# Performance work log

Hardware: AMD Instinct MI355X
Metric: run time of the kernel (lower is better)

## Reference

```python
import jax, jax.numpy as jnp
import numpy as np

B, LAT, H, OUT, S, L = 256, 128, 256, 64, 512, 2


def _lstm_layer(xs, h0, c0, Wih, Whh, bih, bhh):
    # xs: [B, S, in_dim]; PyTorch gate order i, f, g, o
    gx = jnp.einsum('bsi,gi->bsg', xs, Wih) + bih + bhh  # [B,S,4H], precomputed input proj
    gx = jnp.swapaxes(gx, 0, 1)  # [S,B,4H]

    def step(carry, g_t):
        h, c = carry
        g = g_t + h @ Whh.T
        i, f, gg, o = jnp.split(g, 4, axis=-1)
        i, f, o = jax.nn.sigmoid(i), jax.nn.sigmoid(f), jax.nn.sigmoid(o)
        c = f * c + i * jnp.tanh(gg)
        h = o * jnp.tanh(c)
        return (h, c), h

    (_, _), hs = jax.lax.scan(step, (h0, c0), gx)
    return jnp.swapaxes(hs, 0, 1)  # [B,S,H]


def setup_inputs() -> dict:
    key = jax.random.key(0)
    ks = jax.random.split(key, 20)
    sc = 0.05
    d = {
        'z': jax.random.normal(ks[0], (B, LAT), jnp.float32),
        'fc_hidden_w': jax.random.normal(ks[1], (H * L, LAT), jnp.float32) * sc,
        'fc_hidden_b': jnp.zeros((H * L,), jnp.float32),
        'fc_cell_w': jax.random.normal(ks[2], (H * L, LAT), jnp.float32) * sc,
        'fc_cell_b': jnp.zeros((H * L,), jnp.float32),
        'fc_input_w': jax.random.normal(ks[3], (H, LAT), jnp.float32) * sc,
        'fc_input_b': jnp.zeros((H,), jnp.float32),
        'W_ih0': jax.random.normal(ks[4], (4 * H, H), jnp.float32) * sc,
        'W_hh0': jax.random.normal(ks[5], (4 * H, H), jnp.float32) * sc,
        'b_ih0': jnp.zeros((4 * H,), jnp.float32),
        'b_hh0': jnp.zeros((4 * H,), jnp.float32),
        'W_ih1': jax.random.normal(ks[6], (4 * H, H), jnp.float32) * sc,
        'W_hh1': jax.random.normal(ks[7], (4 * H, H), jnp.float32) * sc,
        'b_ih1': jnp.zeros((4 * H,), jnp.float32),
        'b_hh1': jnp.zeros((4 * H,), jnp.float32),
        'fc_output_w': jax.random.normal(ks[8], (OUT, H), jnp.float32) * sc,
        'fc_output_b': jnp.zeros((OUT,), jnp.float32),
    }
    return d


def reference(z, fc_hidden_w, fc_hidden_b, fc_cell_w, fc_cell_b, fc_input_w, fc_input_b,
              W_ih0, W_hh0, b_ih0, b_hh0, W_ih1, W_hh1, b_ih1, b_hh1,
              fc_output_w, fc_output_b):
    # init hidden/cell per layer: view(B, L, H) -> layer axis first
    hidden = (z @ fc_hidden_w.T + fc_hidden_b).reshape(B, L, H)
    cell = (z @ fc_cell_w.T + fc_cell_b).reshape(B, L, H)
    # repeated decoder input (same vector at every timestep)
    x0 = z @ fc_input_w.T + fc_input_b  # [B,H]
    xs = jnp.broadcast_to(x0[:, None, :], (B, S, H))
    h1 = _lstm_layer(xs, hidden[:, 0], cell[:, 0], W_ih0, W_hh0, b_ih0, b_hh0)
    # dropout between layers is inference no-op
    h2 = _lstm_layer(h1, hidden[:, 1], cell[:, 1], W_ih1, W_hh1, b_ih1, b_hh1)
    return h2 @ fc_output_w.T + fc_output_b  # [B,S,OUT]
```

## Files before the change

kernel.cpp:

```cpp
#include <hip/hip_runtime.h>
#include <hip/hip_bf16.h>

#define LAT 128
#define H 256
#define OUTD 64
#define SEQ 512

typedef short bf16x8 __attribute__((ext_vector_type(8)));
typedef float f32x4  __attribute__((ext_vector_type(4)));
typedef unsigned long long u64;
typedef unsigned u32;

__device__ __forceinline__ float sigm(float x)  { return 1.f / (1.f + __expf(-x)); }
__device__ __forceinline__ float tanhf_(float x){ return 1.f - 2.f / (__expf(2.f * x) + 1.f); }

__device__ __forceinline__ short f2bs(float x) {
    __hip_bfloat16 b = __float2bfloat16(x);
    return *reinterpret_cast<short*>(&b);
}
__device__ __forceinline__ float bs2f(unsigned short h) {
    u32 b = ((u32)h) << 16;
    float f; __builtin_memcpy(&f, &b, 4); return f;
}
__device__ __forceinline__ u32 f2pair(float a, float b) {
    return ((u32)(unsigned short)f2bs(b) << 16) | (u32)(unsigned short)f2bs(a);
}
__device__ __forceinline__ bf16x8 pack8(const float* s) {
    bf16x8 v;
    v[0]=f2bs(s[0]); v[1]=f2bs(s[1]); v[2]=f2bs(s[2]); v[3]=f2bs(s[3]);
    v[4]=f2bs(s[4]); v[5]=f2bs(s[5]); v[6]=f2bs(s[6]); v[7]=f2bs(s[7]);
    return v;
}

__device__ __forceinline__ u64 sys_load_u64(const u64* p) {
    return __hip_atomic_load((u64*)p, __ATOMIC_RELAXED, __HIP_MEMORY_SCOPE_AGENT);
}
__device__ __forceinline__ void sys_store_u64(u64* p, u64 v) {
    __hip_atomic_store(p, v, __ATOMIC_RELAXED, __HIP_MEMORY_SCOPE_AGENT);
}

__global__ void lstm_prologue_init(const float* __restrict__ z,
                                   const float* __restrict__ Whid,
                                   const float* __restrict__ bhid,
                                   const float* __restrict__ Wcell,
                                   const float* __restrict__ bcell,
                                   const float* __restrict__ bih1,
                                   const float* __restrict__ bhh1,
                                   u64* __restrict__ h0B1,
                                   u64* __restrict__ h1B1,
                                   float* __restrict__ c0,
                                   float* __restrict__ c1,
                                   float* __restrict__ gxb1)
{
    int t = blockIdx.x * 256 + threadIdx.x;
    if (t < 65536) {
        int layer = t >> 15;
        int tt = t & 32767;
        int b = tt >> 7, cp = tt & 127;
        int colA = layer * H + 2 * cp;
        const float* zr = z + b * LAT;
        const float* wA = Whid + colA * LAT;
        const float* wB = wA + LAT;
        float a0 = bhid[colA], a1 = bhid[colA + 1];
        for (int k = 0; k < LAT; k++) { float zv = zr[k]; a0 += zv * wA[k]; a1 += zv * wB[k]; }
        u64 v = ((u64)(u32)layer << 32) | (u64)f2pair(a0, a1);
        (layer ? h1B1 : h0B1)[b * 128 + cp] = v;
    } else if (t < 196608) {
        int tt = t - 65536;
        int b = tt >> 9, col = tt & 511;
        const float* w  = Wcell + col * LAT;
        const float* zr = z + b * LAT;
        float acc = bcell[col];
        for (int k = 0; k < LAT; k++) acc += zr[k] * w[k];
        if (col < H) c0[b * H + col] = acc;
        else         c1[b * H + (col - H)] = acc;
    } else if (t < 197632) {
        int g = t - 196608;
        gxb1[g] = bih1[g] + bhh1[g];
    }
}

__global__ void lstm_prologue_gx0(const float* __restrict__ z,
                                  const float* __restrict__ Win,
                                  const float* __restrict__ bin,
                                  const float* __restrict__ Wih0,
                                  const float* __restrict__ bih0,
                                  const float* __restrict__ bhh0,
                                  u32* __restrict__ gxb0u)
{
    __shared__ float xs[H];
    const int b = blockIdx.y;
    const int tid = threadIdx.x;
    {
        const float* w  = Win + tid * LAT;
        const float* zr = z + b * LAT;
        float acc = bin[tid];
        for (int k = 0; k < LAT; k++) acc += zr[k] * w[k];
        xs[tid] = acc;
    }
    __syncthreads();
    const int cA = blockIdx.x * 512 + 2 * tid;
    const float* wA = Wih0 + cA * H;
    const float* wB = wA + H;
    float a0 = bih0[cA]     + bhh0[cA];
    float a1 = bih0[cA + 1] + bhh0[cA + 1];
    for (int k = 0; k < H; k++) { float xv = xs[k]; a0 += xv * wA[k]; a1 += xv * wB[k]; }
    gxb0u[b * 512 + blockIdx.x * 256 + tid] = f2pair(a0, a1);
}

__global__ __launch_bounds__(256, 1)
void lstm_persistent(const u32* __restrict__ gxb0u, const float* __restrict__ gxb1,
                     const float* __restrict__ c0g, const float* __restrict__ c1g,
                     u64* __restrict__ h0B0, u64* __restrict__ h0B1,
                     u64* __restrict__ h1B0, u64* __restrict__ h1B1,
                     const float* __restrict__ Whh0, const float* __restrict__ Wih1,
                     const float* __restrict__ Whh1, const float* __restrict__ Wout,
                     const float* __restrict__ bout, float* __restrict__ out)
{
    const int wg = blockIdx.x;
    const int bg = wg >> 4;
    const int j  = wg & 15;
    const int tid  = threadIdx.x;
    const int wave = tid >> 6;
    const int q  = (tid >> 4) & 3;
    const int ln = tid & 15;
    const int mycol = j * 16 + wave * 4 + q;
    const int myb   = bg * 16 + ln;

    __shared__ u32 hs0[2][16 * 132];
    __shared__ u32 hs1[2][16 * 132];

    bf16x8 wf[3][8];
    {
        const float* mats[3] = { Whh0, Wih1, Whh1 };
        const int arow = (ln & 3) * H + j * 16 + wave * 4 + (ln >> 2);
        #pragma unroll
        for (int mm = 0; mm < 3; mm++) {
            const float* s = mats[mm] + arow * H;
            #pragma unroll
            for (int kk = 0; kk < 8; kk++) wf[mm][kk] = pack8(s + kk * 32 + q * 8);
        }
    }
    const bool doOut = (j < 4) && (wave == 0);
    bf16x8 wo[8];
    float bor[4] = {0.f, 0.f, 0.f, 0.f};
    if (doOut) {
        const int orow = j * 16 + ln;
        const float* s = Wout + orow * H;
        #pragma unroll
        for (int kk = 0; kk < 8; kk++) wo[kk] = pack8(s + kk * 32 + q * 8);
        #pragma unroll
        for (int r = 0; r < 4; r++) bor[r] = bout[j * 16 + q * 4 + r];
    }

    float gxr0[4], gxr1[4];
    #pragma unroll
    for (int r = 0; r < 4; r++) {
        u32 v = gxb0u[myb * 512 + ((r * 256 + mycol) >> 1)];
        gxr0[r] = bs2f((unsigned short)((mycol & 1) ? (v >> 16) : (v & 0xFFFFu)));
        gxr1[r] = gxb1[r * 256 + mycol];
    }
    float creg0 = c0g[myb * H + mycol];
    float creg1 = c1g[myb * H + mycol];

    u64* A0 = h0B0 + bg * 2048;
    u64* A1 = h0B1 + bg * 2048;
    u64* B0 = h1B0 + bg * 2048;
    u64* B1 = h1B1 + bg * 2048;

    const int pubslot = ln * 128 + j * 8 + wave * 2 + (q >> 1);
    const bool pubLane = ((q & 1) == 0);

    u64 v0[8];
    #pragma unroll
    for (int i = 0; i < 8; i++) v0[i] = sys_load_u64(A1 + i * 256 + tid);

    for (int k = 0; k <= SEQ + 1; k++) {
        const u64* P1 = (k & 1) ? B1 : B0;  u64* C1 = (k & 1) ? B0 : B1;
        u64* C0 = (k & 1) ? A1 : A0;
        const int par = k & 1;

        if (k <= SEQ) {
            const u64* P0 = (k & 1) ? A0 : A1;
            bool ok = true;
            #pragma unroll
            for (int i = 0; i < 8; i++) ok = ok && ((u32)(v0[i] >> 32) == (u32)k);
            int guard = 0;
            while (!ok && guard < 16384) {
                ok = true;
                #pragma unroll
                for (int i = 0; i < 8; i++) v0[i] = sys_load_u64(P0 + i * 256 + tid);
                #pragma unroll
                for (int i = 0; i < 8; i++) ok = ok && ((u32)(v0[i] >> 32) == (u32)k);
                guard++;
            }
            u32* dst = hs0[par];
            #pragma unroll
            for (int i = 0; i < 8; i++) { int s = i * 256 + tid; dst[(s >> 7) * 132 + (s & 127)] = (u32)v0[i]; }
        }
        __syncthreads();

        bf16x8 hb0[8];
        {
            const unsigned short* b0p = (const unsigned short*)hs0[par];
            #pragma unroll
            for (int kk = 0; kk < 8; kk++)
                hb0[kk] = *(const bf16x8*)(b0p + ln * 264 + kk * 32 + q * 8);
        }

        u64 v1[8];
        if (k >= 1) {
            #pragma unroll
            for (int i = 0; i < 8; i++) v1[i] = sys_load_u64(P1 + i * 256 + tid);
        }
        __builtin_amdgcn_sched_barrier(0);

        if (k < SEQ) {
            f32x4 acc = {0.f, 0.f, 0.f, 0.f};
            #pragma unroll
            for (int kk = 0; kk < 8; kk++)
                acc = __builtin_amdgcn_mfma_f32_16x16x32_bf16(wf[0][kk], hb0[kk], acc, 0, 0, 0);
            float i_ = sigm(acc[0] + gxr0[0]);
            float f_ = sigm(acc[1] + gxr0[1]);
            float g_ = tanhf_(acc[2] + gxr0[2]);
            float o_ = sigm(acc[3] + gxr0[3]);
            creg0 = f_ * creg0 + i_ * g_;
            int us = (int)(u32)(unsigned short)f2bs(o_ * tanhf_(creg0));
            int other = __shfl_xor(us, 16);
            if (pubLane) {
                u32 pa = (u32)us | ((u32)other << 16);
                sys_store_u64(C0 + pubslot, ((u64)(u32)(k + 1) << 32) | (u64)pa);
            }
        }

        if (k >= 1) {
            bool ok = true;
            #pragma unroll
            for (int i = 0; i < 8; i++) ok = ok && ((u32)(v1[i] >> 32) == (u32)k);
            int guard = 0;
            while (!ok && guard < 16384) {
                ok = true;
                #pragma unroll
                for (int i = 0; i < 8; i++) v1[i] = sys_load_u64(P1 + i * 256 + tid);
                #pragma unroll
                for (int i = 0; i < 8; i++) ok = ok && ((u32)(v1[i] >> 32) == (u32)k);
                guard++;
            }
            u32* dst = hs1[par];
            #pragma unroll
            for (int i = 0; i < 8; i++) { int s = i * 256 + tid; dst[(s >> 7) * 132 + (s & 127)] = (u32)v1[i]; }
        }
        __syncthreads();

        bf16x8 hb1[8];
        {
            const unsigned short* b1p = (const unsigned short*)hs1[par];
            #pragma unroll
            for (int kk = 0; kk < 8; kk++)
                hb1[kk] = *(const bf16x8*)(b1p + ln * 264 + kk * 32 + q * 8);
        }

        u32 pa1 = 0; bool pub1 = false;
        if (k >= 1 && k <= SEQ) {
            f32x4 accA = {0.f, 0.f, 0.f, 0.f};
            f32x4 accB = {0.f, 0.f, 0.f, 0.f};
            #pragma unroll
            for (int kk = 0; kk < 8; kk++) {
                accA = __builtin_amdgcn_mfma_f32_16x16x32_bf16(wf[1][kk], hb0[kk], accA, 0, 0, 0);
                accB = __builtin_amdgcn_mfma_f32_16x16x32_bf16(wf[2][kk], hb1[kk], accB, 0, 0, 0);
            }
            float i_ = sigm(accA[0] + accB[0] + gxr1[0]);
            float f_ = sigm(accA[1] + accB[1] + gxr1[1]);
            float g_ = tanhf_(accA[2] + accB[2] + gxr1[2]);
            float o_ = sigm(accA[3] + accB[3] + gxr1[3]);
            creg1 = f_ * creg1 + i_ * g_;
            int us = (int)(u32)(unsigned short)f2bs(o_ * tanhf_(creg1));
            int other = __shfl_xor(us, 16);
            pa1 = (u32)us | ((u32)other << 16);
            pub1 = pubLane;
        }

        if (k < SEQ) {
            #pragma unroll
            for (int i = 0; i < 8; i++) v0[i] = sys_load_u64(C0 + i * 256 + tid);
        }
        __builtin_amdgcn_sched_barrier(0);

        if (pub1) {
            sys_store_u64(C1 + pubslot, ((u64)(u32)(k + 1) << 32) | (u64)pa1);
        }

        if (k >= 2 && doOut) {
            f32x4 acc = {0.f, 0.f, 0.f, 0.f};
            #pragma unroll
            for (int kk = 0; kk < 8; kk++)
                acc = __builtin_amdgcn_mfma_f32_16x16x32_bf16(wo[kk], hb1[kk], acc, 0, 0, 0);
            f32x4 res;
            #pragma unroll
            for (int r = 0; r < 4; r++) res[r] = acc[r] + bor[r];
            *(f32x4*)&out[(bg * 16 + ln) * (SEQ * OUTD) + (k - 2) * OUTD + j * 16 + q * 4] = res;
        }
    }
}

extern "C" void kernel_launch(void* const* d_in, const int* in_sizes, int n_in,
                              void* d_out, int out_size, void* d_ws, size_t ws_size,
                              hipStream_t stream) {
    const float* z     = (const float*)d_in[0];
    const float* Whid  = (const float*)d_in[1];
    const float* bhid  = (const float*)d_in[2];
    const float* Wcell = (const float*)d_in[3];
    const float* bcell = (const float*)d_in[4];
    const float* Win   = (const float*)d_in[5];
    const float* bin   = (const float*)d_in[6];
    const float* Wih0  = (const float*)d_in[7];
    const float* Whh0  = (const float*)d_in[8];
    const float* bih0  = (const float*)d_in[9];
    const float* bhh0  = (const float*)d_in[10];
    const float* Wih1  = (const float*)d_in[11];
    const float* Whh1  = (const float*)d_in[12];
    const float* bih1  = (const float*)d_in[13];
    const float* bhh1  = (const float*)d_in[14];
    const float* Wout  = (const float*)d_in[15];
    const float* bout  = (const float*)d_in[16];
    float* out = (float*)d_out;

    u32*   gxb0u = (u32*)d_ws;
    float* gxb1  = (float*)(gxb0u + 131072);
    float* c0    = gxb1 + 1024;
    float* c1    = c0 + 65536;
    u64*   h0B0  = (u64*)(c1 + 65536);
    u64*   h0B1  = h0B0 + 32768;
    u64*   h1B0  = h0B1 + 32768;
    u64*   h1B1  = h1B0 + 32768;

    lstm_prologue_init<<<772, 256, 0, stream>>>(z, Whid, bhid, Wcell, bcell,
                                                bih1, bhh1, h0B1, h1B1, c0, c1, gxb1);
    lstm_prologue_gx0<<<dim3(2, 256), 256, 0, stream>>>(z, Win, bin, Wih0, bih0, bhh0, gxb0u);

    void* kargs[] = { (void*)&gxb0u, (void*)&gxb1, (void*)&c0, (void*)&c1,
                      (void*)&h0B0, (void*)&h0B1, (void*)&h1B0, (void*)&h1B1,
                      (void*)&Whh0, (void*)&Wih1, (void*)&Whh1, (void*)&Wout,
                      (void*)&bout, (void*)&out };
    hipError_t ce = hipLaunchCooperativeKernel((const void*)lstm_persistent,
                                               dim3(256), dim3(256), kargs, 0, stream);
    if (ce != hipSuccess) {
        lstm_persistent<<<256, 256, 0, stream>>>(gxb0u, gxb1, c0, c1,
                                                 h0B0, h0B1, h1B0, h1B1,
                                                 Whh0, Wih1, Whh1, Wout, bout, out);
    }
}
```

Baseline: 1.499 ms.

## Halve persistent LSTM workgroups, each computing 32 hidden columns per step

Each workgroup of the persistent recurrent kernel now owns 32 hidden columns instead of 16. It holds two sets of weight fragments, issues two MFMA chains per layer and publishes two packed h slots per lane. The grid drops from 256 to 128 workgroups, so each batch group has 8 participants in the per-step flag exchange instead of 16. The aim is to cut cross-workgroup synchronisation and polling traffic, since every workgroup still polls the full h vector each step. The cost is more MFMA and activation work on each step's critical path, higher register pressure, and only half the CUs in use.

```diff
diff --git a/kernel.cpp b/kernel.cpp
--- a/kernel.cpp
+++ b/kernel.cpp
@@ -118,27 +118,29 @@
                      const float* __restrict__ bout, float* __restrict__ out)
 {
     const int wg = blockIdx.x;
-    const int bg = wg >> 4;
-    const int j  = wg & 15;
+    const int bg = wg >> 3;
+    const int j  = wg & 7;
     const int tid  = threadIdx.x;
     const int wave = tid >> 6;
     const int q  = (tid >> 4) & 3;
     const int ln = tid & 15;
-    const int mycol = j * 16 + wave * 4 + q;
     const int myb   = bg * 16 + ln;
 
     __shared__ u32 hs0[2][16 * 132];
     __shared__ u32 hs1[2][16 * 132];
 
-    bf16x8 wf[3][8];
+    bf16x8 wf[3][2][8];
     {
         const float* mats[3] = { Whh0, Wih1, Whh1 };
-        const int arow = (ln & 3) * H + j * 16 + wave * 4 + (ln >> 2);
         #pragma unroll
         for (int mm = 0; mm < 3; mm++) {
-            const float* s = mats[mm] + arow * H;
-            #pragma unroll
-            for (int kk = 0; kk < 8; kk++) wf[mm][kk] = pack8(s + kk * 32 + q * 8);
+            #pragma unroll
+            for (int t = 0; t < 2; t++) {
+                const int arow = (ln & 3) * H + j * 32 + wave * 8 + t * 4 + (ln >> 2);
+                const float* s = mats[mm] + arow * H;
+                #pragma unroll
+                for (int kk = 0; kk < 8; kk++) wf[mm][t][kk] = pack8(s + kk * 32 + q * 8);
+            }
         }
     }
     const bool doOut = (j < 4) && (wave == 0);
@@ -153,22 +155,27 @@
         for (int r = 0; r < 4; r++) bor[r] = bout[j * 16 + q * 4 + r];
     }
 
-    float gxr0[4], gxr1[4];
+    float gxr0[2][4], gxr1[2][4];
+    float creg0[2], creg1[2];
     #pragma unroll
-    for (int r = 0; r < 4; r++) {
-        u32 v = gxb0u[myb * 512 + ((r * 256 + mycol) >> 1)];
-        gxr0[r] = bs2f((unsigned short)((mycol & 1) ? (v >> 16) : (v & 0xFFFFu)));
-        gxr1[r] = gxb1[r * 256 + mycol];
-    }
-    float creg0 = c0g[myb * H + mycol];
-    float creg1 = c1g[myb * H + mycol];
+    for (int t = 0; t < 2; t++) {
+        const int colt = j * 32 + wave * 8 + t * 4 + q;
+        #pragma unroll
+        for (int r = 0; r < 4; r++) {
+            u32 v = gxb0u[myb * 512 + ((r * 256 + colt) >> 1)];
+            gxr0[t][r] = bs2f((unsigned short)((colt & 1) ? (v >> 16) : (v & 0xFFFFu)));
+            gxr1[t][r] = gxb1[r * 256 + colt];
+        }
+        creg0[t] = c0g[myb * H + colt];
+        creg1[t] = c1g[myb * H + colt];
+    }
 
     u64* A0 = h0B0 + bg * 2048;
     u64* A1 = h0B1 + bg * 2048;
     u64* B0 = h1B0 + bg * 2048;
     u64* B1 = h1B1 + bg * 2048;
 
-    const int pubslot = ln * 128 + j * 8 + wave * 2 + (q >> 1);
+    const int pubbase = ln * 128 + j * 16 + wave * 4 + (q >> 1);
     const bool pubLane = ((q & 1) == 0);
 
     u64 v0[8];
@@ -216,20 +223,29 @@
         __builtin_amdgcn_sched_barrier(0);
 
         if (k < SEQ) {
-            f32x4 acc = {0.f, 0.f, 0.f, 0.f};
-            #pragma unroll
-            for (int kk = 0; kk < 8; kk++)
-                acc = __builtin_amdgcn_mfma_f32_16x16x32_bf16(wf[0][kk], hb0[kk], acc, 0, 0, 0);
-            float i_ = sigm(acc[0] + gxr0[0]);
-            float f_ = sigm(acc[1] + gxr0[1]);
-            float g_ = tanhf_(acc[2] + gxr0[2]);
-            float o_ = sigm(acc[3] + gxr0[3]);
-            creg0 = f_ * creg0 + i_ * g_;
-            int us = (int)(u32)(unsigned short)f2bs(o_ * tanhf_(creg0));
-            int other = __shfl_xor(us, 16);
+            f32x4 acc0 = {0.f, 0.f, 0.f, 0.f};
+            f32x4 acc1 = {0.f, 0.f, 0.f, 0.f};
+            #pragma unroll
+            for (int kk = 0; kk < 8; kk++) {
+                acc0 = __builtin_amdgcn_mfma_f32_16x16x32_bf16(wf[0][0][kk], hb0[kk], acc0, 0, 0, 0);
+                acc1 = __builtin_amdgcn_mfma_f32_16x16x32_bf16(wf[0][1][kk], hb0[kk], acc1, 0, 0, 0);
+            }
+            u32 pa[2];
+            #pragma unroll
+            for (int t = 0; t < 2; t++) {
+                const f32x4 acc = t ? acc1 : acc0;
+                float i_ = sigm(acc[0] + gxr0[t][0]);
+                float f_ = sigm(acc[1] + gxr0[t][1]);
+                float g_ = tanhf_(acc[2] + gxr0[t][2]);
+                float o_ = sigm(acc[3] + gxr0[t][3]);
+                creg0[t] = f_ * creg0[t] + i_ * g_;
+                int us = (int)(u32)(unsigned short)f2bs(o_ * tanhf_(creg0[t]));
+                int other = __shfl_xor(us, 16);
+                pa[t] = (u32)us | ((u32)other << 16);
+            }
             if (pubLane) {
-                u32 pa = (u32)us | ((u32)other << 16);
-                sys_store_u64(C0 + pubslot, ((u64)(u32)(k + 1) << 32) | (u64)pa);
+                sys_store_u64(C0 + pubbase + 0, ((u64)(u32)(k + 1) << 32) | (u64)pa[0]);
+                sys_store_u64(C0 + pubbase + 2, ((u64)(u32)(k + 1) << 32) | (u64)pa[1]);
             }
         }
 
@@ -260,23 +276,32 @@
                 hb1[kk] = *(const bf16x8*)(b1p + ln * 264 + kk * 32 + q * 8);
         }
 
-        u32 pa1 = 0; bool pub1 = false;
+        u32 pa1[2]; bool pub1 = false;
         if (k >= 1 && k <= SEQ) {
-            f32x4 accA = {0.f, 0.f, 0.f, 0.f};
-            f32x4 accB = {0.f, 0.f, 0.f, 0.f};
+            f32x4 accA0 = {0.f, 0.f, 0.f, 0.f};
+            f32x4 accB0 = {0.f, 0.f, 0.f, 0.f};
+            f32x4 accA1 = {0.f, 0.f, 0.f, 0.f};
+            f32x4 accB1 = {0.f, 0.f, 0.f, 0.f};
             #pragma unroll
             for (int kk = 0; kk < 8; kk++) {
-                accA = __builtin_amdgcn_mfma_f32_16x16x32_bf16(wf[1][kk], hb0[kk], accA, 0, 0, 0);
-                accB = __builtin_amdgcn_mfma_f32_16x16x32_bf16(wf[2][kk], hb1[kk], accB, 0, 0, 0);
-            }
-            float i_ = sigm(accA[0] + accB[0] + gxr1[0]);
-            float f_ = sigm(accA[1] + accB[1] + gxr1[1]);
-            float g_ = tanhf_(accA[2] + accB[2] + gxr1[2]);
-            float o_ = sigm(accA[3] + accB[3] + gxr1[3]);
-            creg1 = f_ * creg1 + i_ * g_;
-            int us = (int)(u32)(unsigned short)f2bs(o_ * tanhf_(creg1));
-            int other = __shfl_xor(us, 16);
-            pa1 = (u32)us | ((u32)other << 16);
+                accA0 = __builtin_amdgcn_mfma_f32_16x16x32_bf16(wf[1][0][kk], hb0[kk], accA0, 0, 0, 0);
+                accB0 = __builtin_amdgcn_mfma_f32_16x16x32_bf16(wf[2][0][kk], hb1[kk], accB0, 0, 0, 0);
+                accA1 = __builtin_amdgcn_mfma_f32_16x16x32_bf16(wf[1][1][kk], hb0[kk], accA1, 0, 0, 0);
+                accB1 = __builtin_amdgcn_mfma_f32_16x16x32_bf16(wf[2][1][kk], hb1[kk], accB1, 0, 0, 0);
+            }
+            #pragma unroll
+            for (int t = 0; t < 2; t++) {
+                const f32x4 aA = t ? accA1 : accA0;
+                const f32x4 aB = t ? accB1 : accB0;
+                float i_ = sigm(aA[0] + aB[0] + gxr1[t][0]);
+                float f_ = sigm(aA[1] + aB[1] + gxr1[t][1]);
+                float g_ = tanhf_(aA[2] + aB[2] + gxr1[t][2]);
+                float o_ = sigm(aA[3] + aB[3] + gxr1[t][3]);
+                creg1[t] = f_ * creg1[t] + i_ * g_;
+                int us = (int)(u32)(unsigned short)f2bs(o_ * tanhf_(creg1[t]));
+                int other = __shfl_xor(us, 16);
+                pa1[t] = (u32)us | ((u32)other << 16);
+            }
             pub1 = pubLane;
         }
 
@@ -287,7 +312,8 @@
         __builtin_amdgcn_sched_barrier(0);
 
         if (pub1) {
-            sys_store_u64(C1 + pubslot, ((u64)(u32)(k + 1) << 32) | (u64)pa1);
+            sys_store_u64(C1 + pubbase + 0, ((u64)(u32)(k + 1) << 32) | (u64)pa1[0]);
+            sys_store_u64(C1 + pubbase + 2, ((u64)(u32)(k + 1) << 32) | (u64)pa1[1]);
         }
 
         if (k >= 2 && doOut) {
@@ -343,9 +369,9 @@
                       (void*)&Whh0, (void*)&Wih1, (void*)&Whh1, (void*)&Wout,
                       (void*)&bout, (void*)&out };
     hipError_t ce = hipLaunchCooperativeKernel((const void*)lstm_persistent,
-                                               dim3(256), dim3(256), kargs, 0, stream);
+                                               dim3(128), dim3(256), kargs, 0, stream);
     if (ce != hipSuccess) {
-        lstm_persistent<<<256, 256, 0, stream>>>(gxb0u, gxb1, c0, c1,
+        lstm_persistent<<<128, 256, 0, stream>>>(gxb0u, gxb1, c0, c1,
                                                  h0B0, h0B1, h1B0, h1B1,
                                                  Whh0, Wih1, Whh1, Wout, bout, out);
     }
```

Result: slower. 2.084 ms (+39.0%).
